# Optimization experiments

Measured on AMD Instinct MI355X. Metric: run time of the kernel, lower is better.

Reference implementation:

```python
import jax, jax.numpy as jnp
import numpy as np
import math

N = 6000      # nodes
E = 96000     # edges
HID = 32      # hidden_dim
DEPTH = 3
RATIO = 0.2
BN_EPS = 1e-5


def _gcn(x, A, W, b):
    # GCNConv(improved=True): A_hat = A + 2I, out = D^-1/2 A_hat D^-1/2 (x W) + b
    # A[i, j] = weight of edge j -> i (message-passing orientation)
    n = A.shape[0]
    idx = jnp.arange(n)
    Ah = A.at[idx, idx].add(2.0)
    deg = Ah.sum(axis=1)
    dinv = jnp.where(deg > 0, jax.lax.rsqrt(deg), 0.0)
    An = dinv[:, None] * Ah * dinv[None, :]
    return An @ (x @ W) + b


def _two_hop(A):
    # GraphUNet.augment_adj: add self loops, sparse A@A, remove self loops
    n = A.shape[0]
    idx = jnp.arange(n)
    A1 = A.at[idx, idx].add(1.0)
    A2 = A1 @ A1
    return A2.at[idx, idx].set(0.0)


def _unpack(fl):
    x = fl[0]
    wd = list(fl[1:9:2]); bd = list(fl[2:9:2])
    pv = list(fl[9:12])
    wu = list(fl[12:18:2]); bu = list(fl[13:18:2])
    return x, (wd, bd, pv, wu, bu, fl[18], fl[19])


def _forward(x, edge_index, params):
    wd, bd, pv, wu, bu, bn_g, bn_b = params
    n = x.shape[0]
    # dense adjacency, transposed so A[dst, src] = edge weight
    A = jnp.zeros((n, n), x.dtype).at[edge_index[1], edge_index[0]].add(1.0)
    h = jax.nn.relu(_gcn(x, A, wd[0], bd[0]))
    xs, As, perms = [h], [A], []
    Acur = A
    for i in range(DEPTH):
        A2 = _two_hop(Acur)
        # TopKPooling: score = tanh(x.p / ||p||), keep top ceil(ratio*n)
        p = pv[i]
        score = jnp.tanh((h @ p) / jnp.linalg.norm(p))
        k = math.ceil(RATIO * h.shape[0])
        vals, perm = jax.lax.top_k(score, k)
        h = h[perm] * vals[:, None]
        Acur = A2[perm][:, perm]
        h = jax.nn.relu(_gcn(h, Acur, wd[i + 1], bd[i + 1]))
        if i < DEPTH - 1:
            xs.append(h)
            As.append(Acur)
        perms.append(perm)
    for i in range(DEPTH):
        j = DEPTH - 1 - i
        up = jnp.zeros_like(xs[j]).at[perms[j]].set(h)  # unpool
        h = _gcn(xs[j] + up, As[j], wu[i], bu[i])       # sum_res=True
        if i < DEPTH - 1:
            h = jax.nn.relu(h)
    # PFNet5 tail: BatchNorm1d(1) (batch stats) + sigmoid on channel 0
    v = h[:, 0]
    mean = v.mean()
    var = jnp.mean((v - mean) ** 2)
    r1 = jax.nn.sigmoid(bn_g[0] * (v - mean) * jax.lax.rsqrt(var + BN_EPS) + bn_b[0])
    return h.at[:, 0].set(r1)


def setup_inputs() -> dict:
    key = jax.random.key(0)
    ks = jax.random.split(key, 20)
    def nrm(k, shape, s=0.1):
        return jax.random.normal(k, shape, jnp.float32) * s
    inp = {
        "x": jax.random.normal(ks[0], (N, 3), jnp.float32),
        "edge_index": jax.random.randint(ks[1], (2, E), 0, N),
    }
    dims_down = [(3, HID), (HID, HID), (HID, HID), (HID, HID)]
    for i, (di, do) in enumerate(dims_down):
        inp[f"w_down{i}"] = nrm(ks[2 + i], (di, do))
        inp[f"b_down{i}"] = jnp.zeros((do,), jnp.float32)
    for i in range(3):
        inp[f"pool{i}"] = nrm(ks[6 + i], (HID,))
    dims_up = [(HID, HID), (HID, HID), (HID, 4)]
    for i, (di, do) in enumerate(dims_up):
        inp[f"w_up{i}"] = nrm(ks[9 + i], (di, do))
        inp[f"b_up{i}"] = jnp.zeros((do,), jnp.float32)
    inp["bn_gamma"] = jnp.ones((1,), jnp.float32)
    inp["bn_beta"] = jnp.zeros((1,), jnp.float32)
    return inp


def reference(x, edge_index, w_down0, b_down0, w_down1, b_down1, w_down2, b_down2,
              w_down3, b_down3, pool0, pool1, pool2, w_up0, b_up0, w_up1, b_up1,
              w_up2, b_up2, bn_gamma, bn_beta):
    fl = (x, w_down0, b_down0, w_down1, b_down1, w_down2, b_down2, w_down3, b_down3,
          pool0, pool1, pool2, w_up0, b_up0, w_up1, b_up1, w_up2, b_up2,
          bn_gamma, bn_beta)
    x_, params = _unpack(fl)
    return _forward(x_, edge_index, params)
```

## Files before the change

### kernel.cpp

```cpp
#include <hip/hip_runtime.h>
#include <hip/hip_bf16.h>

#define TPB 256

__global__ void k_count(const int* __restrict__ ei, int E, int* __restrict__ cnt){
  int e = blockIdx.x*blockDim.x + threadIdx.x;
  if(e < E) atomicAdd(&cnt[ei[E + e]], 1);
}

template<int IPT>
__global__ void k_scan(const int* __restrict__ cnt, int n, int* __restrict__ rowptr){
  int tid = threadIdx.x;
  int base = tid * IPT;
  int loc[IPT]; int s = 0;
  #pragma unroll
  for(int q = 0; q < IPT; ++q){ int i = base + q; int v = (i < n) ? cnt[i] : 0; s += v; loc[q] = s; }
  int lane = tid & 63, w = tid >> 6;
  int ss = s;
  #pragma unroll
  for(int o = 1; o < 64; o <<= 1){ int t = __shfl_up(ss, o, 64); if(lane >= o) ss += t; }
  __shared__ int wsum[16];
  if(lane == 63) wsum[w] = ss;
  __syncthreads();
  if(tid < 16){
    int t = wsum[tid];
    for(int o = 1; o < 16; o <<= 1){ int u = __shfl_up(t, o, 64); if(tid >= o) t += u; }
    wsum[tid] = t;
  }
  __syncthreads();
  int excl = ss - s + (w > 0 ? wsum[w-1] : 0);
  if(tid == 0) rowptr[0] = 0;
  #pragma unroll
  for(int q = 0; q < IPT; ++q){ int i = base + q; if(i < n) rowptr[i+1] = excl + loc[q]; }
}

__global__ void k_fill(const int* __restrict__ ei, int E, const int* __restrict__ rowptr,
                       int* __restrict__ fill, int* __restrict__ colidx){
  int e = blockIdx.x*blockDim.x + threadIdx.x;
  if(e >= E) return;
  int d = ei[E + e], s = ei[e];
  int p = rowptr[d] + atomicAdd(&fill[d], 1);
  colidx[p] = s;
}

__global__ void k_mm_dinv(const float* __restrict__ h, const float* __restrict__ W,
                          const float* __restrict__ dinv, const int* __restrict__ cnt,
                          float* __restrict__ dinv_out, float* __restrict__ out,
                          int n, int cin, int cout){
  int t = blockIdx.x*blockDim.x + threadIdx.x;
  if(t >= n*cout) return;
  int i = t / cout, c = t - i*cout;
  float dv;
  if(cnt){ dv = rsqrtf((float)cnt[i] + 2.0f); if(c == 0) dinv_out[i] = dv; }
  else dv = dinv[i];
  float s = 0.f;
  for(int d = 0; d < cin; ++d) s += h[i*cin + d] * W[d*cout + c];
  out[t] = dv * s;
}

template<int COUT>
__global__ void k_addup_mm(const float* __restrict__ base, const float* __restrict__ h,
                           const int* __restrict__ rank, const float* __restrict__ W,
                           const float* __restrict__ dinv, float* __restrict__ out, int n){
  int t = blockIdx.x*blockDim.x + threadIdx.x;
  if(t >= n*COUT) return;
  int i = t / COUT, c = t - i*COUT;
  int r = rank[i];
  const float* br = base + (size_t)i*32;
  const float* hr = h + (size_t)(r >= 0 ? r : 0)*32;
  float s = 0.f;
  #pragma unroll
  for(int d = 0; d < 32; ++d){
    float z = br[d] + ((r >= 0) ? hr[d] : 0.f);
    s += z * W[d*COUT + c];
  }
  out[t] = dinv[i] * s;
}

template<int C, bool RELU, bool SCORE>
__global__ void k_csr_gcn(const int* __restrict__ rowptr, const int* __restrict__ colidx,
                          const float* __restrict__ xwd, const float* __restrict__ dinv,
                          const float* __restrict__ bias, float* __restrict__ out, int n,
                          const float* __restrict__ pvec, float* __restrict__ score){
  int t = blockIdx.x*blockDim.x + threadIdx.x;
  if(t >= n*C) return;
  int i = t / C, c = t % C;
  float acc = 2.0f * xwd[i*C + c];
  int b = rowptr[i], e = rowptr[i+1];
  for(int p = b; p < e; ++p) acc += xwd[colidx[p]*C + c];
  float y = dinv[i]*acc + bias[c];
  y = RELU ? fmaxf(y, 0.f) : y;
  out[t] = y;
  if(SCORE){
    float pv = pvec[c];
    float sd = y*pv, nn = pv*pv;
    #pragma unroll
    for(int o = 16; o > 0; o >>= 1){ sd += __shfl_xor(sd, o, 32); nn += __shfl_xor(nn, o, 32); }
    if(c == 0) score[i] = tanhf(sd / sqrtf(nn));
  }
}

template<int NMAX>
__global__ __launch_bounds__(1024)
void k_pool_radix(const float* __restrict__ score, const float* __restrict__ h,
                  int n, int k, int* __restrict__ perm, int* __restrict__ rank,
                  float* __restrict__ hout){
  __shared__ unsigned keys[NMAX];
  __shared__ int bins[2048];
  __shared__ int wsum[16];
  __shared__ unsigned s_prefix;
  __shared__ int s_rk, s_found, s_cntgt;
  int tid = threadIdx.x, lane = tid & 63, w = tid >> 6;

  for(int i = tid; i < n; i += 1024){
    rank[i] = -1;
    unsigned u = __float_as_uint(score[i]);
    u ^= (u & 0x80000000u) ? 0xFFFFFFFFu : 0x80000000u;
    keys[i] = u;
  }
  if(tid == 0){ s_prefix = 0u; s_rk = k; }
  __syncthreads();

  for(int pass = 0; pass < 3; ++pass){
    const int width = (pass < 2) ? 11 : 10;
    const int shift = (pass == 0) ? 21 : ((pass == 1) ? 10 : 0);
    const int nb = 1 << width;
    for(int b2 = tid; b2 < nb; b2 += 1024) bins[b2] = 0;
    __syncthreads();
    unsigned prefix = s_prefix;
    int rk = s_rk;
    const int hs = shift + width;
    for(int i = tid; i < n; i += 1024){
      unsigned kk = keys[i];
      bool match = (pass == 0) || ((kk >> hs) == (prefix >> hs));
      if(match) atomicAdd(&bins[(kk >> shift) & (nb-1)], 1);
    }
    __syncthreads();
    int ipt = (nb + 1023) >> 10;
    int loc0 = 0, loc1 = 0, s = 0;
    { int r = tid*ipt; int v = (r < nb) ? bins[nb-1-r] : 0; s += v; loc0 = s;
      if(ipt == 2){ int r2 = r+1; int v2 = (r2 < nb) ? bins[nb-1-r2] : 0; s += v2; loc1 = s; } }
    int ss = s;
    #pragma unroll
    for(int o = 1; o < 64; o <<= 1){ int t2 = __shfl_up(ss, o, 64); if(lane >= o) ss += t2; }
    if(lane == 63) wsum[w] = ss;
    __syncthreads();
    if(tid < 16){
      int t2 = wsum[tid];
      #pragma unroll
      for(int o = 1; o < 16; o <<= 1){ int u2 = __shfl_up(t2, o, 64); if(tid >= o) t2 += u2; }
      wsum[tid] = t2;
    }
    __syncthreads();
    int excl = ss - s + (w ? wsum[w-1] : 0);
    { int r = tid*ipt; if(r < nb) bins[nb-1-r] = excl + loc0;
      if(ipt == 2){ int r2 = r+1; if(r2 < nb) bins[nb-1-r2] = excl + loc1; } }
    __syncthreads();
    for(int b2 = tid; b2 < nb; b2 += 1024){
      int cge = bins[b2];
      int cgt = (b2+1 < nb) ? bins[b2+1] : 0;
      if(cge >= rk && cgt < rk){ s_found = b2; s_cntgt = cgt; }
    }
    __syncthreads();
    if(tid == 0){ s_prefix |= ((unsigned)s_found) << shift; s_rk -= s_cntgt; }
    __syncthreads();
  }
  unsigned T = s_prefix;
  int r = s_rk;
  int cgt_total = k - r;

  int CH = (n + 1023) >> 10;
  int base = tid*CH, c_gt = 0, c_eq = 0;
  for(int q = 0; q < CH; ++q){
    int i = base+q;
    if(i < n){ unsigned u = keys[i]; c_gt += (u > T); c_eq += (u == T); }
  }
  int packed = c_gt*8192 + c_eq;
  int ss2 = packed;
  #pragma unroll
  for(int o = 1; o < 64; o <<= 1){ int t2 = __shfl_up(ss2, o, 64); if(lane >= o) ss2 += t2; }
  if(lane == 63) wsum[w] = ss2;
  __syncthreads();
  if(tid < 16){
    int t2 = wsum[tid];
    #pragma unroll
    for(int o = 1; o < 16; o <<= 1){ int u2 = __shfl_up(t2, o, 64); if(tid >= o) t2 += u2; }
    wsum[tid] = t2;
  }
  __syncthreads();
  int excl2 = ss2 - packed + (w ? wsum[w-1] : 0);
  int gt_before = excl2 / 8192, eq_before = excl2 % 8192;
  for(int q = 0; q < CH; ++q){
    int i = base+q;
    if(i >= n) continue;
    unsigned u = keys[i];
    if(u > T){ int pos = gt_before++; perm[pos] = i; rank[i] = pos; }
    else if(u == T){
      int tr = eq_before++;
      if(tr < r){ int pos = cgt_total + tr; perm[pos] = i; rank[i] = pos; }
    }
  }
  __syncthreads();
  for(int t = tid; t < k*32; t += 1024){
    int i = t >> 5, c = t & 31;
    int idx = perm[i];
    hout[t] = h[(size_t)idx*32 + c] * score[idx];
  }
}

__global__ __launch_bounds__(256)
void k_build_B1(const int* __restrict__ rowptr, const int* __restrict__ colidx,
                const int* __restrict__ perm1, const int* __restrict__ rank1, int K1,
                float* __restrict__ dinv1, int* __restrict__ rowbeg, int* __restrict__ rowend,
                int* __restrict__ col1, float* __restrict__ val1, int* __restrict__ cursor){
  __shared__ float row[1216];
  __shared__ int wsum[4];
  __shared__ float fs[4];
  __shared__ int s_base;
  int tid = threadIdx.x, lane = tid & 63, w = tid >> 6;
  int i = blockIdx.x;
  for(int j = tid; j < K1; j += 256) row[j] = 0.f;
  __syncthreads();
  int d = perm1[i];
  int b = rowptr[d], len = rowptr[d+1]-b;
  for(int p = tid; p < len; p += 256){
    int s = colidx[b+p]; int rs = rank1[s];
    if(rs >= 0) atomicAdd(&row[rs], 2.0f);
  }
  for(int ww = tid; ww < len*8; ww += 256){
    int p = ww >> 3, sub = ww & 7;
    int s = colidx[b+p];
    for(int q = rowptr[s]+sub, qe = rowptr[s+1]; q < qe; q += 8){
      int r2 = rank1[colidx[q]];
      if(r2 >= 0) atomicAdd(&row[r2], 1.0f);
    }
  }
  __syncthreads();
  if(tid == 0) row[i] = 0.f;
  __syncthreads();
  float s = 0.f;
  for(int j = tid; j < K1; j += 256) s += row[j];
  for(int o = 32; o > 0; o >>= 1) s += __shfl_down(s, o, 64);
  if(lane == 0) fs[w] = s;
  __syncthreads();
  if(tid == 0){
    dinv1[i] = rsqrtf(fs[0]+fs[1]+fs[2]+fs[3] + 2.0f);
    row[i] = 1.0f;
  }
  __syncthreads();
  int CH = (K1 + 255) >> 8;
  int base = tid*CH, cnt = 0;
  for(int q = 0; q < CH; ++q){ int j = base+q; if(j < K1 && row[j] != 0.f) ++cnt; }
  int ss = cnt;
  #pragma unroll
  for(int o = 1; o < 64; o <<= 1){ int t2 = __shfl_up(ss, o, 64); if(lane >= o) ss += t2; }
  if(lane == 63) wsum[w] = ss;
  __syncthreads();
  if(tid < 4){
    int t2 = wsum[tid];
    for(int o = 1; o < 4; o <<= 1){ int u2 = __shfl_up(t2, o, 64); if(tid >= o) t2 += u2; }
    wsum[tid] = t2;
  }
  __syncthreads();
  if(tid == 0) s_base = atomicAdd(cursor, wsum[3]);
  __syncthreads();
  int off = s_base + ss - cnt + (w ? wsum[w-1] : 0);
  for(int q = 0; q < CH; ++q){
    int j = base+q;
    if(j < K1 && row[j] != 0.f){ col1[off] = j; val1[off] = row[j]; ++off; }
  }
  if(tid == 0){ rowbeg[i] = s_base; rowend[i] = s_base + wsum[3]; }
}

template<bool RELU, bool SCORE>
__global__ void k_spmm_gcn(const int* __restrict__ rb, const int* __restrict__ re,
                           const int* __restrict__ ci, const float* __restrict__ cv,
                           const float* __restrict__ hwd, const float* __restrict__ dinv,
                           const float* __restrict__ bias, float* __restrict__ out, int n,
                           const float* __restrict__ pvec, float* __restrict__ score){
  int t = blockIdx.x*blockDim.x + threadIdx.x;
  if(t >= n*32) return;
  int i = t >> 5, c = t & 31;
  float acc = hwd[i*32 + c];
  for(int p = rb[i], e = re[i]; p < e; ++p) acc += cv[p]*hwd[ci[p]*32 + c];
  float y = dinv[i]*acc + bias[c];
  y = RELU ? fmaxf(y, 0.f) : y;
  out[t] = y;
  if(SCORE){
    float pv = pvec[c];
    float sd = y*pv, nn = pv*pv;
    #pragma unroll
    for(int o = 16; o > 0; o >>= 1){ sd += __shfl_xor(sd, o, 32); nn += __shfl_xor(nn, o, 32); }
    if(c == 0) score[i] = tanhf(sd / sqrtf(nn));
  }
}

__global__ __launch_bounds__(256)
void k_twohop_sp(const int* __restrict__ rb, const int* __restrict__ re,
                 const int* __restrict__ ci, const float* __restrict__ cv,
                 const int* __restrict__ perm2, const int* __restrict__ rank2,
                 float* __restrict__ C2, float* __restrict__ dinv2, int K2){
  __shared__ float acc[256];
  __shared__ float fs[4];
  int i = blockIdx.x, tid = threadIdx.x, lane = tid & 63, w = tid >> 6;
  for(int j = tid; j < K2; j += 256) acc[j] = 0.f;
  __syncthreads();
  int qi = perm2[i];
  int b = rb[qi], len = re[qi]-b;
  for(int ww = tid; ww < len*8; ww += 256){
    int p = b + (ww >> 3), sub = ww & 7;
    int t = ci[p]; float v = cv[p];
    for(int q = rb[t] + sub, qe = re[t]; q < qe; q += 8){
      int j = rank2[ci[q]];
      if(j >= 0) atomicAdd(&acc[j], v*cv[q]);
    }
  }
  __syncthreads();
  if(tid == 0) acc[i] = 0.f;
  __syncthreads();
  float s = 0.f;
  for(int j = tid; j < K2; j += 256) s += acc[j];
  for(int o = 32; o > 0; o >>= 1) s += __shfl_down(s, o, 64);
  if(lane == 0) fs[w] = s;
  __syncthreads();
  if(tid == 0) dinv2[i] = rsqrtf(fs[0]+fs[1]+fs[2]+fs[3] + 2.0f);
  for(int j = tid; j < K2; j += 256) C2[(size_t)i*K2 + j] = acc[j];
}

template<bool RELU, bool SCORE>
__global__ void k_dgcn_row(const float* __restrict__ C, const float* __restrict__ hwd,
                           const float* __restrict__ dinv, const float* __restrict__ bias,
                           float* __restrict__ out, int n,
                           const float* __restrict__ pvec, float* __restrict__ score){
  __shared__ float sh[8][32];
  int i = blockIdx.x;
  int c = threadIdx.x & 31, s = threadIdx.x >> 5;
  const float* row = C + (size_t)i*n;
  float acc = 0.f;
  for(int t = s; t < n; t += 8) acc += row[t]*hwd[t*32 + c];
  sh[s][c] = acc;
  __syncthreads();
  if(s == 0){
    float a = sh[0][c]+sh[1][c]+sh[2][c]+sh[3][c]+sh[4][c]+sh[5][c]+sh[6][c]+sh[7][c];
    a += 2.f*hwd[i*32 + c];
    float y = dinv[i]*a + bias[c];
    y = RELU ? fmaxf(y, 0.f) : y;
    out[i*32 + c] = y;
    if(SCORE){
      float pv = pvec[c];
      float sd = y*pv, nn = pv*pv;
      #pragma unroll
      for(int o = 16; o > 0; o >>= 1){ sd += __shfl_xor(sd, o, 32); nn += __shfl_xor(nn, o, 32); }
      if(c == 0) score[i] = tanhf(sd / sqrtf(nn));
    }
  }
}

__global__ __launch_bounds__(256)
void k_twohop_d3(const float* __restrict__ C2, int n, const int* __restrict__ perm3,
                 int k, float* __restrict__ C3, float* __restrict__ dinv3){
  __shared__ float acc[4][64];
  int i = blockIdx.x, tid = threadIdx.x;
  int col = tid & 63, st = tid >> 6;
  int qi = perm3[i];
  int qj = (col < k) ? perm3[col] : 0;
  float a = 0.f;
  if(col < k){
    for(int tt = st; tt < n; tt += 4){
      float av = C2[(size_t)qi*n + tt] + ((tt == qi) ? 1.f : 0.f);
      float bv = C2[(size_t)tt*n + qj] + ((tt == qj) ? 1.f : 0.f);
      a += av * bv;
    }
  }
  acc[st][col] = a;
  __syncthreads();
  if(st == 0){
    float v = acc[0][col]+acc[1][col]+acc[2][col]+acc[3][col];
    if(col == i) v = 0.f;
    if(col < k) C3[(size_t)i*k + col] = v;
    float sv = (col < k) ? v : 0.f;
    for(int o = 32; o > 0; o >>= 1) sv += __shfl_down(sv, o, 64);
    if(col == 0) dinv3[i] = rsqrtf(sv + 2.0f);
  }
}

__global__ void k_bn(float* __restrict__ out, int n, const float* __restrict__ g,
                     const float* __restrict__ b){
  __shared__ float sh[16];
  __shared__ float sval;
  int tid = threadIdx.x, lane = tid & 63, w = tid >> 6;
  int nw = blockDim.x >> 6;
  float s = 0.f;
  for(int i = tid; i < n; i += blockDim.x) s += out[i*4];
  for(int o = 32; o > 0; o >>= 1) s += __shfl_down(s, o, 64);
  if(lane == 0) sh[w] = s;
  __syncthreads();
  if(tid == 0){ float t = 0.f; for(int q = 0; q < nw; ++q) t += sh[q]; sval = t / n; }
  __syncthreads();
  float mean = sval;
  float v = 0.f;
  for(int i = tid; i < n; i += blockDim.x){ float d = out[i*4] - mean; v += d*d; }
  for(int o = 32; o > 0; o >>= 1) v += __shfl_down(v, o, 64);
  __syncthreads();
  if(lane == 0) sh[w] = v;
  __syncthreads();
  if(tid == 0){ float t = 0.f; for(int q = 0; q < nw; ++q) t += sh[q]; sval = t / n; }
  __syncthreads();
  float var = sval;
  float scale = g[0] * rsqrtf(var + 1e-5f);
  float beta = b[0];
  for(int i = tid; i < n; i += blockDim.x){
    float r = scale*(out[i*4] - mean) + beta;
    out[i*4] = 1.f / (1.f + expf(-r));
  }
}

extern "C" void kernel_launch(void* const* d_in, const int* in_sizes, int n_in,
                              void* d_out, int out_size, void* d_ws, size_t ws_size,
                              hipStream_t stream){
  const float* x  =(const float*)d_in[0];
  const int*   ei =(const int*)  d_in[1];
  const float* W0 =(const float*)d_in[2];  const float* b0 =(const float*)d_in[3];
  const float* W1 =(const float*)d_in[4];  const float* b1 =(const float*)d_in[5];
  const float* W2 =(const float*)d_in[6];  const float* b2 =(const float*)d_in[7];
  const float* W3 =(const float*)d_in[8];  const float* b3 =(const float*)d_in[9];
  const float* p0 =(const float*)d_in[10];
  const float* p1 =(const float*)d_in[11];
  const float* p2 =(const float*)d_in[12];
  const float* Wu0=(const float*)d_in[13]; const float* bu0=(const float*)d_in[14];
  const float* Wu1=(const float*)d_in[15]; const float* bu1=(const float*)d_in[16];
  const float* Wu2=(const float*)d_in[17]; const float* bu2=(const float*)d_in[18];
  const float* bng=(const float*)d_in[19]; const float* bnb=(const float*)d_in[20];
  float* out = (float*)d_out;

  const int n0 = in_sizes[0] / 3;
  const int E  = in_sizes[1] / 2;
  const int K1 = (n0 + 4) / 5;
  const int K2 = (K1 + 4) / 5;
  const int K3 = (K2 + 4) / 5;
  const int CAP1 = 512*1024;

  char* wsp = (char*)d_ws; size_t off = 0;
  auto alloc = [&](size_t bytes)->char*{
    char* p = wsp + off; off = (off + bytes + 255) & ~((size_t)255); return p;
  };

  int*   zreg   = (int*)  alloc((size_t)(2*n0+64)*4);
  int*   cnt    = zreg;
  int*   fill   = zreg + n0;
  int*   cursor = zreg + 2*n0;
  int*   rowptr = (int*)  alloc((size_t)(n0+1)*4);
  int*   colidx = (int*)  alloc((size_t)E*4);
  float* dinv0  = (float*)alloc((size_t)n0*4);
  float* hwd    = (float*)alloc((size_t)n0*32*4);
  float* h0     = (float*)alloc((size_t)n0*32*4);
  float* score  = (float*)alloc((size_t)n0*4);
  int*   perm1  = (int*)  alloc((size_t)K1*4);
  int*   rank1  = (int*)  alloc((size_t)n0*4);
  float* h1p    = (float*)alloc((size_t)K1*32*4);
  float* dinv1  = (float*)alloc((size_t)K1*4);
  int*   rowbeg1= (int*)  alloc((size_t)K1*4);
  int*   rowend1= (int*)  alloc((size_t)K1*4);
  int*   col1   = (int*)  alloc((size_t)CAP1*4);
  float* val1   = (float*)alloc((size_t)CAP1*4);
  float* h1     = (float*)alloc((size_t)K1*32*4);
  int*   perm2  = (int*)  alloc((size_t)K2*4);
  int*   rank2  = (int*)  alloc((size_t)K1*4);
  float* h2p    = (float*)alloc((size_t)K2*32*4);
  float* C2     = (float*)alloc((size_t)K2*K2*4);
  float* dinv2  = (float*)alloc((size_t)K2*4);
  float* h2     = (float*)alloc((size_t)K2*32*4);
  int*   perm3  = (int*)  alloc((size_t)K3*4);
  int*   rank3  = (int*)  alloc((size_t)K2*4);
  float* h3p    = (float*)alloc((size_t)K3*32*4);
  float* C3     = (float*)alloc((size_t)K3*K3*4);
  float* dinv3  = (float*)alloc((size_t)K3*4);
  float* h3     = (float*)alloc((size_t)K3*32*4);
  float* hu2    = (float*)alloc((size_t)K2*32*4);
  float* hu1    = (float*)alloc((size_t)K1*32*4);

  hipMemsetAsync(zreg, 0, (size_t)(2*n0+64)*4, stream);

  const int gE = (E + TPB - 1) / TPB;
  k_count  <<<gE, TPB, 0, stream>>>(ei, E, cnt);
  k_scan<6><<<1, 1024, 0, stream>>>(cnt, n0, rowptr);
  k_fill   <<<gE, TPB, 0, stream>>>(ei, E, rowptr, fill, colidx);
  k_mm_dinv<<<(n0*32+TPB-1)/TPB, TPB, 0, stream>>>(x, W0, nullptr, cnt, dinv0, hwd, n0, 3, 32);
  k_csr_gcn<32,true,true><<<(n0*32+TPB-1)/TPB, TPB, 0, stream>>>(rowptr, colidx, hwd, dinv0, b0, h0, n0, p0, score);
  k_pool_radix<6144><<<1, 1024, 0, stream>>>(score, h0, n0, K1, perm1, rank1, h1p);
  k_build_B1<<<K1, 256, 0, stream>>>(rowptr, colidx, perm1, rank1, K1,
                                     dinv1, rowbeg1, rowend1, col1, val1, cursor);
  k_mm_dinv<<<(K1*32+TPB-1)/TPB, TPB, 0, stream>>>(h1p, W1, dinv1, nullptr, nullptr, hwd, K1, 32, 32);
  k_spmm_gcn<true,true><<<(K1*32+TPB-1)/TPB, TPB, 0, stream>>>(rowbeg1, rowend1, col1, val1, hwd, dinv1, b1, h1, K1, p1, score);
  k_pool_radix<1216><<<1, 1024, 0, stream>>>(score, h1, K1, K2, perm2, rank2, h2p);
  k_twohop_sp<<<K2, 256, 0, stream>>>(rowbeg1, rowend1, col1, val1, perm2, rank2, C2, dinv2, K2);
  k_mm_dinv<<<(K2*32+TPB-1)/TPB, TPB, 0, stream>>>(h2p, W2, dinv2, nullptr, nullptr, hwd, K2, 32, 32);
  k_dgcn_row<true,true><<<K2, 256, 0, stream>>>(C2, hwd, dinv2, b2, h2, K2, p2, score);
  k_pool_radix<256><<<1, 1024, 0, stream>>>(score, h2, K2, K3, perm3, rank3, h3p);
  k_twohop_d3<<<K3, 256, 0, stream>>>(C2, K2, perm3, K3, C3, dinv3);
  k_mm_dinv<<<(K3*32+TPB-1)/TPB, TPB, 0, stream>>>(h3p, W3, dinv3, nullptr, nullptr, hwd, K3, 32, 32);
  k_dgcn_row<true,false><<<K3, 256, 0, stream>>>(C3, hwd, dinv3, b3, h3, K3, nullptr, nullptr);
  k_addup_mm<32><<<(K2*32+TPB-1)/TPB, TPB, 0, stream>>>(h2, h3, rank3, Wu0, dinv2, hwd, K2);
  k_dgcn_row<true,false><<<K2, 256, 0, stream>>>(C2, hwd, dinv2, bu0, hu2, K2, nullptr, nullptr);
  k_addup_mm<32><<<(K1*32+TPB-1)/TPB, TPB, 0, stream>>>(h1, hu2, rank2, Wu1, dinv1, hwd, K1);
  k_spmm_gcn<true,false><<<(K1*32+TPB-1)/TPB, TPB, 0, stream>>>(rowbeg1, rowend1, col1, val1, hwd, dinv1, bu1, hu1, K1, nullptr, nullptr);
  k_addup_mm<4><<<(n0*4+TPB-1)/TPB, TPB, 0, stream>>>(h0, hu1, rank1, Wu2, dinv0, hwd, n0);
  k_csr_gcn<4,false,false><<<(n0*4+TPB-1)/TPB, TPB, 0, stream>>>(rowptr, colidx, hwd, dinv0, bu2, out, n0, nullptr, nullptr);
  k_bn<<<1, 1024, 0, stream>>>(out, n0, bng, bnb);
}
```

Measured before the change: 246.1 us.

## Fuse whole GraphUNet pipeline into one cooperative persistent kernel with grid syncs

Replaces the chain of about twenty kernel launches with a single cooperative kernel of 240 blocks that runs every stage, separated by grid.sync(). It also reorders some arithmetic: the first GCN aggregates the 3-wide input before multiplying by W0, and the last layer projects to 4 channels before aggregating. The pooled-feature gather is fused with the weight multiply, and batch norm is folded into block partial sums. This removes launch overhead, but the top-k pools run on a single 256-thread block while the rest of the grid waits, and the many grid barriers carry their own cost.

```diff
diff --git a/kernel.cpp b/kernel.cpp
--- a/kernel.cpp
+++ b/kernel.cpp
@@ -1,7 +1,444 @@
 #include <hip/hip_runtime.h>
+#include <hip/hip_cooperative_groups.h>
 #include <hip/hip_bf16.h>
 
+namespace cg = cooperative_groups;
+
 #define TPB 256
+#define GRID 240
+
+__device__ __forceinline__ int incl_scan256(int v, int* wsum){
+  int tid = threadIdx.x, lane = tid & 63, w = tid >> 6;
+  int ss = v;
+  #pragma unroll
+  for(int o = 1; o < 64; o <<= 1){ int t = __shfl_up(ss, o, 64); if(lane >= o) ss += t; }
+  __syncthreads();
+  if(lane == 63) wsum[w] = ss;
+  __syncthreads();
+  if(tid < 4){
+    int t = wsum[tid];
+    #pragma unroll
+    for(int o = 1; o < 4; o <<= 1){ int uu = __shfl_up(t, o, 64); if(tid >= o) t += uu; }
+    wsum[tid] = t;
+  }
+  __syncthreads();
+  return ss + (w ? wsum[w-1] : 0);
+}
+
+__device__ __forceinline__ float block_sum_f(float v, float* fs){
+  int tid = threadIdx.x, lane = tid & 63, w = tid >> 6;
+  #pragma unroll
+  for(int o = 32; o > 0; o >>= 1) v += __shfl_down(v, o, 64);
+  __syncthreads();
+  if(lane == 0) fs[w] = v;
+  __syncthreads();
+  return fs[0] + fs[1] + fs[2] + fs[3];
+}
+
+__device__ void pool256(const float* __restrict__ score, int n, int k,
+                        int* __restrict__ perm, int* __restrict__ rank,
+                        unsigned* keys, int* bins, int* wsum,
+                        unsigned* s_pref, int* s_rk, int* s_found, int* s_cg){
+  int tid = threadIdx.x;
+  for(int i = tid; i < n; i += 256){
+    unsigned uu = __float_as_uint(score[i]);
+    uu ^= (uu & 0x80000000u) ? 0xFFFFFFFFu : 0x80000000u;
+    keys[i] = uu;
+  }
+  if(tid == 0){ *s_pref = 0u; *s_rk = k; }
+  __syncthreads();
+  for(int pass = 0; pass < 3; ++pass){
+    const int width = (pass < 2) ? 11 : 10;
+    const int shift = (pass == 0) ? 21 : ((pass == 1) ? 10 : 0);
+    const int nb = 1 << width;
+    for(int b = tid; b < nb; b += 256) bins[b] = 0;
+    __syncthreads();
+    unsigned prefix = *s_pref; int rk = *s_rk;
+    const int hs = shift + width;
+    for(int i = tid; i < n; i += 256){
+      unsigned kk = keys[i];
+      bool match = (pass == 0) || ((kk >> hs) == (prefix >> hs));
+      if(match) atomicAdd(&bins[(kk >> shift) & (nb-1)], 1);
+    }
+    __syncthreads();
+    const int ipt = nb >> 8;
+    int loc[8]; int s = 0;
+    for(int q = 0; q < ipt; ++q){ int rr = tid*ipt + q; s += bins[nb-1-rr]; loc[q] = s; }
+    int incl = incl_scan256(s, wsum);
+    int excl = incl - s;
+    for(int q = 0; q < ipt; ++q){ int rr = tid*ipt + q; bins[nb-1-rr] = excl + loc[q]; }
+    __syncthreads();
+    for(int b = tid; b < nb; b += 256){
+      int cge = bins[b], cgt = (b+1 < nb) ? bins[b+1] : 0;
+      if(cge >= rk && cgt < rk){ *s_found = b; *s_cg = cgt; }
+    }
+    __syncthreads();
+    if(tid == 0){ *s_pref |= ((unsigned)(*s_found)) << shift; *s_rk = rk - (*s_cg); }
+    __syncthreads();
+  }
+  unsigned T = *s_pref; int r = *s_rk; int cgt_total = k - r;
+  int CH = (n + 255) >> 8;
+  int base = tid*CH, c_gt = 0, c_eq = 0;
+  for(int q = 0; q < CH; ++q){
+    int i = base + q;
+    if(i < n){ unsigned uu = keys[i]; c_gt += (uu > T); c_eq += (uu == T); }
+  }
+  int packed = c_gt*8192 + c_eq;
+  int incl2 = incl_scan256(packed, wsum);
+  int excl2 = incl2 - packed;
+  int gt_b = excl2 / 8192, eq_b = excl2 % 8192;
+  for(int q = 0; q < CH; ++q){
+    int i = base + q; if(i >= n) continue;
+    unsigned uu = keys[i];
+    if(uu > T){ int pos = gt_b++; perm[pos] = i; rank[i] = pos; }
+    else if(uu == T){ int tr = eq_b++; if(tr < r){ int pos = cgt_total + tr; perm[pos] = i; rank[i] = pos; } }
+  }
+}
+
+struct GP {
+  const float* x; const int* ei;
+  const float *W0,*b0,*W1,*b1,*W2,*b2,*W3,*b3;
+  const float *p0,*p1,*p2;
+  const float *Wu0,*bu0,*Wu1,*bu1,*Wu2,*bu2,*bng,*bnb;
+  float* out;
+  int n0, E, K1, K2, K3;
+  int *cnt,*fillc,*cursor,*rowptr,*colidx;
+  float *dinv0,*xa,*h0,*score;
+  int *perm1,*rank1;
+  float *hw1,*dinv1; int *rowbeg1,*rowend1,*col1; float *val1;
+  float *h1; int *perm2,*rank2; float *hw2,*C2,*dinv2,*h2;
+  int *perm3,*rank3; float *hw3,*C3,*dinv3,*h3;
+  float *hu2,*hu1,*hw4,*bnp,*bnq;
+};
+
+union SMem {
+  struct { unsigned keys[6144]; int bins[2048]; } pool;
+  float row[1216];
+  float acc[256];
+  float sh[8][32];
+  float acc3[4][64];
+};
+
+__global__ __launch_bounds__(256)
+void k_mega(GP p){
+  cg::grid_group grid = cg::this_grid();
+  __shared__ SMem u;
+  __shared__ int wsum[16];
+  __shared__ unsigned s_pref;
+  __shared__ int s_rk, s_found, s_cg, s_base;
+  __shared__ float fs[4];
+  const int tid = threadIdx.x, bid = blockIdx.x;
+  const int gsz = gridDim.x * blockDim.x, gtid = bid*blockDim.x + tid;
+  const int n0 = p.n0, E = p.E, K1 = p.K1, K2 = p.K2, K3 = p.K3;
+
+  for(int i = gtid; i < n0; i += gsz){ p.cnt[i] = 0; p.fillc[i] = 0; }
+  if(gtid == 0) *p.cursor = 0;
+  grid.sync();
+  for(int e = gtid; e < E; e += gsz) atomicAdd(&p.cnt[p.ei[E + e]], 1);
+  grid.sync();
+  if(bid == 0){
+    const int IPT = 24;
+    int base = tid*IPT, loc[IPT], s = 0;
+    for(int q = 0; q < IPT; ++q){ int i = base + q; int v = (i < n0) ? p.cnt[i] : 0; s += v; loc[q] = s; }
+    int incl = incl_scan256(s, wsum);
+    int excl = incl - s;
+    if(tid == 0) p.rowptr[0] = 0;
+    for(int q = 0; q < IPT; ++q){ int i = base + q; if(i < n0) p.rowptr[i+1] = excl + loc[q]; }
+  }
+  grid.sync();
+  for(int e = gtid; e < E; e += gsz){
+    int d = p.ei[E + e], s = p.ei[e];
+    int pos = p.rowptr[d] + atomicAdd(&p.fillc[d], 1);
+    p.colidx[pos] = s;
+  }
+  grid.sync();
+  for(int i = gtid; i < n0; i += gsz){
+    float di = rsqrtf((float)p.cnt[i] + 2.0f);
+    p.dinv0[i] = di;
+    float s0 = 2.f*di*p.x[i*3], s1 = 2.f*di*p.x[i*3+1], s2 = 2.f*di*p.x[i*3+2];
+    for(int q = p.rowptr[i]; q < p.rowptr[i+1]; ++q){
+      int j = p.colidx[q];
+      float dj = rsqrtf((float)p.cnt[j] + 2.0f);
+      s0 += dj*p.x[j*3]; s1 += dj*p.x[j*3+1]; s2 += dj*p.x[j*3+2];
+    }
+    p.xa[i*3] = s0; p.xa[i*3+1] = s1; p.xa[i*3+2] = s2;
+    p.rank1[i] = -1;
+  }
+  grid.sync();
+  for(int t = gtid; t < n0*32; t += gsz){
+    int i = t >> 5, c = t & 31;
+    float y = p.dinv0[i]*(p.xa[i*3]*p.W0[c] + p.xa[i*3+1]*p.W0[32+c] + p.xa[i*3+2]*p.W0[64+c]) + p.b0[c];
+    y = fmaxf(y, 0.f); p.h0[t] = y;
+    float pv = p.p0[c]; float sd = y*pv, nn = pv*pv;
+    #pragma unroll
+    for(int o = 16; o > 0; o >>= 1){ sd += __shfl_xor(sd, o, 32); nn += __shfl_xor(nn, o, 32); }
+    if(c == 0) p.score[i] = tanhf(sd / sqrtf(nn));
+  }
+  grid.sync();
+  if(bid == 0) pool256(p.score, n0, K1, p.perm1, p.rank1, u.pool.keys, u.pool.bins, wsum, &s_pref, &s_rk, &s_found, &s_cg);
+  grid.sync();
+  for(int t = gtid; t < K1*32; t += gsz){
+    int i = t >> 5, c = t & 31; int idx = p.perm1[i]; float sc = p.score[idx];
+    const float* hr = p.h0 + (size_t)idx*32;
+    float s = 0.f;
+    #pragma unroll
+    for(int d = 0; d < 32; ++d) s += hr[d]*p.W1[d*32 + c];
+    p.hw1[t] = sc*s;
+  }
+  for(int i = bid; i < K1; i += gridDim.x){
+    for(int j = tid; j < K1; j += 256) u.row[j] = 0.f;
+    __syncthreads();
+    int d = p.perm1[i];
+    int b = p.rowptr[d], len = p.rowptr[d+1] - b;
+    for(int q = tid; q < len; q += 256){
+      int s = p.colidx[b + q]; int rs = p.rank1[s];
+      if(rs >= 0) atomicAdd(&u.row[rs], 2.0f);
+    }
+    for(int ww = tid; ww < len*8; ww += 256){
+      int q = ww >> 3, sub = ww & 7;
+      int s = p.colidx[b + q];
+      for(int e2 = p.rowptr[s] + sub, ee = p.rowptr[s+1]; e2 < ee; e2 += 8){
+        int r2 = p.rank1[p.colidx[e2]];
+        if(r2 >= 0) atomicAdd(&u.row[r2], 1.0f);
+      }
+    }
+    __syncthreads();
+    if(tid == 0) u.row[i] = 0.f;
+    __syncthreads();
+    float s = 0.f;
+    for(int j = tid; j < K1; j += 256) s += u.row[j];
+    float tot = block_sum_f(s, fs);
+    if(tid == 0){ p.dinv1[i] = rsqrtf(tot + 2.0f); u.row[i] = 1.0f; }
+    __syncthreads();
+    const int CH = (1200 + 255) >> 8;
+    int base = tid*CH, cnt2 = 0;
+    for(int q = 0; q < CH; ++q){ int j = base + q; if(j < K1 && u.row[j] != 0.f) ++cnt2; }
+    int incl = incl_scan256(cnt2, wsum);
+    if(tid == 255) s_base = atomicAdd(p.cursor, incl);
+    __syncthreads();
+    int off = s_base + (incl - cnt2);
+    for(int q = 0; q < CH; ++q){
+      int j = base + q;
+      if(j < K1 && u.row[j] != 0.f){ p.col1[off] = j; p.val1[off] = u.row[j]; ++off; }
+    }
+    if(tid == 0)   p.rowbeg1[i] = s_base;
+    if(tid == 255) p.rowend1[i] = s_base + incl;
+    __syncthreads();
+  }
+  grid.sync();
+  for(int i = gtid; i < K1; i += gsz) p.rank2[i] = -1;
+  for(int t = gtid; t < K1*32; t += gsz){
+    int i = t >> 5, c = t & 31;
+    float acc = p.dinv1[i]*p.hw1[t];
+    for(int q = p.rowbeg1[i]; q < p.rowend1[i]; ++q){
+      int j = p.col1[q];
+      acc += p.val1[q]*p.dinv1[j]*p.hw1[j*32 + c];
+    }
+    float y = p.dinv1[i]*acc + p.b1[c];
+    y = fmaxf(y, 0.f); p.h1[t] = y;
+    float pv = p.p1[c]; float sd = y*pv, nn = pv*pv;
+    #pragma unroll
+    for(int o = 16; o > 0; o >>= 1){ sd += __shfl_xor(sd, o, 32); nn += __shfl_xor(nn, o, 32); }
+    if(c == 0) p.score[i] = tanhf(sd / sqrtf(nn));
+  }
+  grid.sync();
+  if(bid == 0) pool256(p.score, K1, K2, p.perm2, p.rank2, u.pool.keys, u.pool.bins, wsum, &s_pref, &s_rk, &s_found, &s_cg);
+  grid.sync();
+  for(int t = gtid; t < K2*32; t += gsz){
+    int i = t >> 5, c = t & 31; int idx = p.perm2[i]; float sc = p.score[idx];
+    const float* hr = p.h1 + (size_t)idx*32;
+    float s = 0.f;
+    #pragma unroll
+    for(int d = 0; d < 32; ++d) s += hr[d]*p.W2[d*32 + c];
+    p.hw2[t] = sc*s;
+  }
+  for(int i = bid; i < K2; i += gridDim.x){
+    for(int j = tid; j < K2; j += 256) u.acc[j] = 0.f;
+    __syncthreads();
+    int qi = p.perm2[i];
+    int b = p.rowbeg1[qi], len = p.rowend1[qi] - b;
+    for(int ww = tid; ww < len*8; ww += 256){
+      int q = b + (ww >> 3), sub = ww & 7;
+      int t2 = p.col1[q]; float v = p.val1[q];
+      for(int e2 = p.rowbeg1[t2] + sub, ee = p.rowend1[t2]; e2 < ee; e2 += 8){
+        int j = p.rank2[p.col1[e2]];
+        if(j >= 0) atomicAdd(&u.acc[j], v*p.val1[e2]);
+      }
+    }
+    __syncthreads();
+    if(tid == 0) u.acc[i] = 0.f;
+    __syncthreads();
+    float s = 0.f;
+    for(int j = tid; j < K2; j += 256) s += u.acc[j];
+    float tot = block_sum_f(s, fs);
+    if(tid == 0) p.dinv2[i] = rsqrtf(tot + 2.0f);
+    for(int j = tid; j < K2; j += 256) p.C2[(size_t)i*K2 + j] = u.acc[j];
+    __syncthreads();
+  }
+  grid.sync();
+  for(int i = bid; i < K2; i += gridDim.x){
+    int c = tid & 31, sg = tid >> 5;
+    const float* Crow = p.C2 + (size_t)i*K2;
+    float a = 0.f;
+    for(int t2 = sg; t2 < K2; t2 += 8) a += Crow[t2]*p.dinv2[t2]*p.hw2[t2*32 + c];
+    u.sh[sg][c] = a;
+    __syncthreads();
+    if(sg == 0){
+      float aa = u.sh[0][c]+u.sh[1][c]+u.sh[2][c]+u.sh[3][c]+u.sh[4][c]+u.sh[5][c]+u.sh[6][c]+u.sh[7][c];
+      aa += 2.f*p.dinv2[i]*p.hw2[i*32 + c];
+      float y = p.dinv2[i]*aa + p.b2[c];
+      y = fmaxf(y, 0.f);
+      p.h2[i*32 + c] = y;
+      float pv = p.p2[c]; float sd = y*pv, nn = pv*pv;
+      #pragma unroll
+      for(int o = 16; o > 0; o >>= 1){ sd += __shfl_xor(sd, o, 32); nn += __shfl_xor(nn, o, 32); }
+      if(c == 0){ p.score[i] = tanhf(sd / sqrtf(nn)); p.rank3[i] = -1; }
+    }
+    __syncthreads();
+  }
+  grid.sync();
+  if(bid == 0) pool256(p.score, K2, K3, p.perm3, p.rank3, u.pool.keys, u.pool.bins, wsum, &s_pref, &s_rk, &s_found, &s_cg);
+  grid.sync();
+  for(int t = gtid; t < K3*32; t += gsz){
+    int i = t >> 5, c = t & 31; int idx = p.perm3[i]; float sc = p.score[idx];
+    const float* hr = p.h2 + (size_t)idx*32;
+    float s = 0.f;
+    #pragma unroll
+    for(int d = 0; d < 32; ++d) s += hr[d]*p.W3[d*32 + c];
+    p.hw3[t] = sc*s;
+  }
+  if(bid < K3){
+    int i = bid;
+    int col = tid & 63, st = tid >> 6;
+    int qi = p.perm3[i];
+    int qj = (col < K3) ? p.perm3[col] : 0;
+    float a = 0.f;
+    if(col < K3){
+      for(int t2 = st; t2 < K2; t2 += 4){
+        float av = p.C2[(size_t)qi*K2 + t2] + ((t2 == qi) ? 1.f : 0.f);
+        float bv = p.C2[(size_t)t2*K2 + qj] + ((t2 == qj) ? 1.f : 0.f);
+        a += av*bv;
+      }
+    }
+    u.acc3[st][col] = a;
+    __syncthreads();
+    if(st == 0){
+      float v = u.acc3[0][col]+u.acc3[1][col]+u.acc3[2][col]+u.acc3[3][col];
+      if(col == i) v = 0.f;
+      if(col < K3) p.C3[(size_t)i*K3 + col] = v;
+      float sv = (col < K3) ? v : 0.f;
+      #pragma unroll
+      for(int o = 32; o > 0; o >>= 1) sv += __shfl_down(sv, o, 64);
+      if(col == 0) p.dinv3[i] = rsqrtf(sv + 2.0f);
+    }
+  }
+  grid.sync();
+  for(int i = bid; i < K3; i += gridDim.x){
+    int c = tid & 31, sg = tid >> 5;
+    const float* Crow = p.C3 + (size_t)i*K3;
+    float a = 0.f;
+    for(int t2 = sg; t2 < K3; t2 += 8) a += Crow[t2]*p.dinv3[t2]*p.hw3[t2*32 + c];
+    u.sh[sg][c] = a;
+    __syncthreads();
+    if(sg == 0){
+      float aa = u.sh[0][c]+u.sh[1][c]+u.sh[2][c]+u.sh[3][c]+u.sh[4][c]+u.sh[5][c]+u.sh[6][c]+u.sh[7][c];
+      aa += 2.f*p.dinv3[i]*p.hw3[i*32 + c];
+      float y = p.dinv3[i]*aa + p.b3[c];
+      p.h3[i*32 + c] = fmaxf(y, 0.f);
+    }
+    __syncthreads();
+  }
+  grid.sync();
+  for(int t = gtid; t < K2*32; t += gsz){
+    int i = t >> 5, c = t & 31; int r = p.rank3[i];
+    float s = 0.f;
+    #pragma unroll
+    for(int d = 0; d < 32; ++d){
+      float z = p.h2[i*32 + d] + ((r >= 0) ? p.h3[r*32 + d] : 0.f);
+      s += z*p.Wu0[d*32 + c];
+    }
+    p.hw2[t] = s;
+  }
+  grid.sync();
+  for(int i = bid; i < K2; i += gridDim.x){
+    int c = tid & 31, sg = tid >> 5;
+    const float* Crow = p.C2 + (size_t)i*K2;
+    float a = 0.f;
+    for(int t2 = sg; t2 < K2; t2 += 8) a += Crow[t2]*p.dinv2[t2]*p.hw2[t2*32 + c];
+    u.sh[sg][c] = a;
+    __syncthreads();
+    if(sg == 0){
+      float aa = u.sh[0][c]+u.sh[1][c]+u.sh[2][c]+u.sh[3][c]+u.sh[4][c]+u.sh[5][c]+u.sh[6][c]+u.sh[7][c];
+      aa += 2.f*p.dinv2[i]*p.hw2[i*32 + c];
+      float y = p.dinv2[i]*aa + p.bu0[c];
+      p.hu2[i*32 + c] = fmaxf(y, 0.f);
+    }
+    __syncthreads();
+  }
+  grid.sync();
+  for(int t = gtid; t < K1*32; t += gsz){
+    int i = t >> 5, c = t & 31; int r = p.rank2[i];
+    float s = 0.f;
+    #pragma unroll
+    for(int d = 0; d < 32; ++d){
+      float z = p.h1[i*32 + d] + ((r >= 0) ? p.hu2[r*32 + d] : 0.f);
+      s += z*p.Wu1[d*32 + c];
+    }
+    p.hw1[t] = s;
+  }
+  grid.sync();
+  for(int t = gtid; t < K1*32; t += gsz){
+    int i = t >> 5, c = t & 31;
+    float acc = p.dinv1[i]*p.hw1[t];
+    for(int q = p.rowbeg1[i]; q < p.rowend1[i]; ++q){
+      int j = p.col1[q];
+      acc += p.val1[q]*p.dinv1[j]*p.hw1[j*32 + c];
+    }
+    float y = p.dinv1[i]*acc + p.bu1[c];
+    p.hu1[t] = fmaxf(y, 0.f);
+  }
+  grid.sync();
+  for(int t = gtid; t < n0*4; t += gsz){
+    int i = t >> 2, c = t & 3; int r = p.rank1[i];
+    float s = 0.f;
+    #pragma unroll
+    for(int d = 0; d < 32; ++d){
+      float z = p.h0[i*32 + d] + ((r >= 0) ? p.hu1[r*32 + d] : 0.f);
+      s += z*p.Wu2[d*4 + c];
+    }
+    p.hw4[t] = p.dinv0[i]*s;
+  }
+  grid.sync();
+  {
+    float vs = 0.f, vq = 0.f;
+    for(int t = gtid; t < n0*4; t += gsz){
+      int i = t >> 2, c = t & 3;
+      float acc = 2.f*p.hw4[t];
+      for(int q = p.rowptr[i]; q < p.rowptr[i+1]; ++q) acc += p.hw4[p.colidx[q]*4 + c];
+      float y = p.dinv0[i]*acc + p.bu2[c];
+      p.out[t] = y;
+      if(c == 0){ vs += y; vq += y*y; }
+    }
+    float bs = block_sum_f(vs, fs);
+    float bq = block_sum_f(vq, fs);
+    if(tid == 0){ p.bnp[bid] = bs; p.bnq[bid] = bq; }
+  }
+  grid.sync();
+  {
+    float sv = (tid < (int)gridDim.x) ? p.bnp[tid] : 0.f;
+    float qv = (tid < (int)gridDim.x) ? p.bnq[tid] : 0.f;
+    float tsum = block_sum_f(sv, fs);
+    float tsq  = block_sum_f(qv, fs);
+    float mean = tsum / n0;
+    float var  = tsq / n0 - mean*mean;
+    float scale = p.bng[0]*rsqrtf(var + 1e-5f);
+    float beta  = p.bnb[0];
+    for(int i = gtid; i < n0; i += gsz){
+      float r = scale*(p.out[i*4] - mean) + beta;
+      p.out[i*4] = 1.f/(1.f + expf(-r));
+    }
+  }
+}
 
 __global__ void k_count(const int* __restrict__ ei, int E, int* __restrict__ cnt){
   int e = blockIdx.x*blockDim.x + threadIdx.x;
@@ -24,7 +461,7 @@
   __syncthreads();
   if(tid < 16){
     int t = wsum[tid];
-    for(int o = 1; o < 16; o <<= 1){ int u = __shfl_up(t, o, 64); if(tid >= o) t += u; }
+    for(int o = 1; o < 16; o <<= 1){ int uu = __shfl_up(t, o, 64); if(tid >= o) t += uu; }
     wsum[tid] = t;
   }
   __syncthreads();
@@ -111,16 +548,14 @@
   __shared__ unsigned s_prefix;
   __shared__ int s_rk, s_found, s_cntgt;
   int tid = threadIdx.x, lane = tid & 63, w = tid >> 6;
-
   for(int i = tid; i < n; i += 1024){
     rank[i] = -1;
-    unsigned u = __float_as_uint(score[i]);
-    u ^= (u & 0x80000000u) ? 0xFFFFFFFFu : 0x80000000u;
-    keys[i] = u;
+    unsigned uu = __float_as_uint(score[i]);
+    uu ^= (uu & 0x80000000u) ? 0xFFFFFFFFu : 0x80000000u;
+    keys[i] = uu;
   }
   if(tid == 0){ s_prefix = 0u; s_rk = k; }
   __syncthreads();
-
   for(int pass = 0; pass < 3; ++pass){
     const int width = (pass < 2) ? 11 : 10;
     const int shift = (pass == 0) ? 21 : ((pass == 1) ? 10 : 0);
@@ -168,12 +603,11 @@
   unsigned T = s_prefix;
   int r = s_rk;
   int cgt_total = k - r;
-
   int CH = (n + 1023) >> 10;
   int base = tid*CH, c_gt = 0, c_eq = 0;
   for(int q = 0; q < CH; ++q){
     int i = base+q;
-    if(i < n){ unsigned u = keys[i]; c_gt += (u > T); c_eq += (u == T); }
+    if(i < n){ unsigned uu = keys[i]; c_gt += (uu > T); c_eq += (uu == T); }
   }
   int packed = c_gt*8192 + c_eq;
   int ss2 = packed;
@@ -193,9 +627,9 @@
   for(int q = 0; q < CH; ++q){
     int i = base+q;
     if(i >= n) continue;
-    unsigned u = keys[i];
-    if(u > T){ int pos = gt_before++; perm[pos] = i; rank[i] = pos; }
-    else if(u == T){
+    unsigned uu = keys[i];
+    if(uu > T){ int pos = gt_before++; perm[pos] = i; rank[i] = pos; }
+    else if(uu == T){
       int tr = eq_before++;
       if(tr < r){ int pos = cgt_total + tr; perm[pos] = i; rank[i] = pos; }
     }
@@ -379,6 +813,7 @@
     if(col == i) v = 0.f;
     if(col < k) C3[(size_t)i*k + col] = v;
     float sv = (col < k) ? v : 0.f;
+    #pragma unroll
     for(int o = 32; o > 0; o >>= 1) sv += __shfl_down(sv, o, 64);
     if(col == 0) dinv3[i] = rsqrtf(sv + 2.0f);
   }
@@ -447,17 +882,19 @@
 
   int*   zreg   = (int*)  alloc((size_t)(2*n0+64)*4);
   int*   cnt    = zreg;
-  int*   fill   = zreg + n0;
+  int*   fillc  = zreg + n0;
   int*   cursor = zreg + 2*n0;
   int*   rowptr = (int*)  alloc((size_t)(n0+1)*4);
   int*   colidx = (int*)  alloc((size_t)E*4);
   float* dinv0  = (float*)alloc((size_t)n0*4);
   float* hwd    = (float*)alloc((size_t)n0*32*4);
+  float* xa     = (float*)alloc((size_t)n0*3*4);
   float* h0     = (float*)alloc((size_t)n0*32*4);
   float* score  = (float*)alloc((size_t)n0*4);
   int*   perm1  = (int*)  alloc((size_t)K1*4);
   int*   rank1  = (int*)  alloc((size_t)n0*4);
   float* h1p    = (float*)alloc((size_t)K1*32*4);
+  float* hw1    = (float*)alloc((size_t)K1*32*4);
   float* dinv1  = (float*)alloc((size_t)K1*4);
   int*   rowbeg1= (int*)  alloc((size_t)K1*4);
   int*   rowend1= (int*)  alloc((size_t)K1*4);
@@ -467,24 +904,49 @@
   int*   perm2  = (int*)  alloc((size_t)K2*4);
   int*   rank2  = (int*)  alloc((size_t)K1*4);
   float* h2p    = (float*)alloc((size_t)K2*32*4);
+  float* hw2    = (float*)alloc((size_t)K2*32*4);
   float* C2     = (float*)alloc((size_t)K2*K2*4);
   float* dinv2  = (float*)alloc((size_t)K2*4);
   float* h2     = (float*)alloc((size_t)K2*32*4);
   int*   perm3  = (int*)  alloc((size_t)K3*4);
   int*   rank3  = (int*)  alloc((size_t)K2*4);
   float* h3p    = (float*)alloc((size_t)K3*32*4);
+  float* hw3    = (float*)alloc((size_t)K3*32*4);
   float* C3     = (float*)alloc((size_t)K3*K3*4);
   float* dinv3  = (float*)alloc((size_t)K3*4);
   float* h3     = (float*)alloc((size_t)K3*32*4);
   float* hu2    = (float*)alloc((size_t)K2*32*4);
   float* hu1    = (float*)alloc((size_t)K1*32*4);
+  float* hw4    = (float*)alloc((size_t)n0*4*4);
+  float* bnp    = (float*)alloc((size_t)256*4);
+  float* bnq    = (float*)alloc((size_t)256*4);
+
+  GP gp;
+  gp.x=x; gp.ei=ei;
+  gp.W0=W0; gp.b0=b0; gp.W1=W1; gp.b1=b1; gp.W2=W2; gp.b2=b2; gp.W3=W3; gp.b3=b3;
+  gp.p0=p0; gp.p1=p1; gp.p2=p2;
+  gp.Wu0=Wu0; gp.bu0=bu0; gp.Wu1=Wu1; gp.bu1=bu1; gp.Wu2=Wu2; gp.bu2=bu2;
+  gp.bng=bng; gp.bnb=bnb;
+  gp.out=out;
+  gp.n0=n0; gp.E=E; gp.K1=K1; gp.K2=K2; gp.K3=K3;
+  gp.cnt=cnt; gp.fillc=fillc; gp.cursor=cursor; gp.rowptr=rowptr; gp.colidx=colidx;
+  gp.dinv0=dinv0; gp.xa=xa; gp.h0=h0; gp.score=score;
+  gp.perm1=perm1; gp.rank1=rank1;
+  gp.hw1=hw1; gp.dinv1=dinv1; gp.rowbeg1=rowbeg1; gp.rowend1=rowend1; gp.col1=col1; gp.val1=val1;
+  gp.h1=h1; gp.perm2=perm2; gp.rank2=rank2; gp.hw2=hw2; gp.C2=C2; gp.dinv2=dinv2; gp.h2=h2;
+  gp.perm3=perm3; gp.rank3=rank3; gp.hw3=hw3; gp.C3=C3; gp.dinv3=dinv3; gp.h3=h3;
+  gp.hu2=hu2; gp.hu1=hu1; gp.hw4=hw4; gp.bnp=bnp; gp.bnq=bnq;
+
+  void* kargs[] = { (void*)&gp };
+  hipError_t err = hipLaunchCooperativeKernel((const void*)k_mega, dim3(GRID), dim3(TPB),
+                                              kargs, 0, stream);
+  if(err == hipSuccess) return;
 
   hipMemsetAsync(zreg, 0, (size_t)(2*n0+64)*4, stream);
-
   const int gE = (E + TPB - 1) / TPB;
   k_count  <<<gE, TPB, 0, stream>>>(ei, E, cnt);
   k_scan<6><<<1, 1024, 0, stream>>>(cnt, n0, rowptr);
-  k_fill   <<<gE, TPB, 0, stream>>>(ei, E, rowptr, fill, colidx);
+  k_fill   <<<gE, TPB, 0, stream>>>(ei, E, rowptr, fillc, colidx);
   k_mm_dinv<<<(n0*32+TPB-1)/TPB, TPB, 0, stream>>>(x, W0, nullptr, cnt, dinv0, hwd, n0, 3, 32);
   k_csr_gcn<32,true,true><<<(n0*32+TPB-1)/TPB, TPB, 0, stream>>>(rowptr, colidx, hwd, dinv0, b0, h0, n0, p0, score);
   k_pool_radix<6144><<<1, 1024, 0, stream>>>(score, h0, n0, K1, perm1, rank1, h1p);
```

Measured after the change: 709.8 us. 188% more time.
